# Performance work log

Hardware: AMD Instinct MI355X
Metric: run time of the kernel (lower is better)

## Reference

```python
import jax, jax.numpy as jnp
import numpy as np

HIDDEN = 1024
HEADS = 16
HEAD_DIM = HIDDEN // HEADS


def setup_inputs() -> dict:
    key = jax.random.key(0)
    ks = jax.random.split(key, 4)
    B, S, H = 2, 2048, HIDDEN
    scale = 1.0 / np.sqrt(H)
    return {
        "inputs": jax.random.normal(ks[0], (B, S, H), dtype=jnp.float32),
        "mask": jnp.ones((B, S), dtype=jnp.int32),
        "Wq": jax.random.normal(ks[1], (H, H), dtype=jnp.float32) * scale,
        "bq": jnp.zeros((H,), dtype=jnp.float32),
        "Wk": jax.random.normal(ks[2], (H, H), dtype=jnp.float32) * scale,
        "bk": jnp.zeros((H,), dtype=jnp.float32),
        "Wv": jax.random.normal(ks[3], (H, H), dtype=jnp.float32) * scale,
        "bv": jnp.zeros((H,), dtype=jnp.float32),
    }


def _split_heads(x, B, S):
    # [B,S,H] -> [B,heads,S,head_dim]
    return x.reshape(B, S, HEADS, HEAD_DIM).transpose(0, 2, 1, 3)


def reference(inputs, mask, Wq, bq, Wk, bk, Wv, bv):
    B, S, H = inputs.shape
    q = _split_heads(inputs @ Wq.T + bq, B, S)
    k = _split_heads(inputs @ Wk.T + bk, B, S)
    v = _split_heads(inputs @ Wv.T + bv, B, S)
    scores = jnp.einsum("bhqd,bhkd->bhqk", q, k) / jnp.sqrt(
        jnp.asarray(HEAD_DIM, dtype=inputs.dtype))
    # mask broadcast [B,1,1,S]; zeros -> -inf
    scores = jnp.where(mask[:, None, None, :] == 0, -jnp.inf, scores)
    attn = jax.nn.softmax(scores, axis=-1)
    context = jnp.einsum("bhqk,bhkd->bhqd", attn, v)
    return context.transpose(0, 2, 1, 3).reshape(B, S, H)
```

## Files before the change

### kernel.cpp

```cpp
#include <hip/hip_runtime.h>
#include <hip/hip_fp16.h>

constexpr int S_LEN  = 2048;
constexpr int HID    = 1024;
constexpr int HEADS  = 16;
constexpr int HDIM   = 64;
constexpr int BATCH  = 2;
constexpr int BH     = BATCH * HEADS;
constexpr int M_ROWS = BATCH * S_LEN;

typedef _Float16 half8  __attribute__((ext_vector_type(8)));
typedef _Float16 half4v __attribute__((ext_vector_type(4)));
typedef _Float16 half2v __attribute__((ext_vector_type(2)));
typedef float    f32x4  __attribute__((ext_vector_type(4)));
typedef float    f32x16 __attribute__((ext_vector_type(16)));
typedef unsigned uint4v __attribute__((ext_vector_type(4)));

constexpr float EXP2_OFF = -11.541560327111707f;
constexpr float Q_SCALE  = 0.18033688011112042f;

__global__ __launch_bounds__(256) void cvt_kernel(
    const float* __restrict__ X,  const float* __restrict__ Wq,
    const float* __restrict__ Wk, const float* __restrict__ Wv,
    const int* __restrict__ mask,
    _Float16* __restrict__ Xh,  _Float16* __restrict__ Wqh,
    _Float16* __restrict__ Wkh, _Float16* __restrict__ Wvh,
    float* __restrict__ maskF)
{
    const int blk = blockIdx.x;
    if (blk >= 3584) {
        const int loc = blk - 3584;
        const size_t e = ((size_t)loc * 256 + threadIdx.x) * 8;
        #pragma unroll
        for (int i = 0; i < 8; ++i)
            maskF[e + i] = mask[e + i] ? EXP2_OFF : -1.0e30f;
        return;
    }
    const float* src; _Float16* dst; int loc;
    if (blk < 2048)      { src = X;  dst = Xh;  loc = blk; }
    else if (blk < 2560) { src = Wq; dst = Wqh; loc = blk - 2048; }
    else if (blk < 3072) { src = Wk; dst = Wkh; loc = blk - 2560; }
    else                 { src = Wv; dst = Wvh; loc = blk - 3072; }
    const size_t e = ((size_t)loc * 256 + threadIdx.x) * 8;
    float4 a = *reinterpret_cast<const float4*>(&src[e]);
    float4 b = *reinterpret_cast<const float4*>(&src[e + 4]);
    half8 h = { (_Float16)a.x, (_Float16)a.y, (_Float16)a.z, (_Float16)a.w,
                (_Float16)b.x, (_Float16)b.y, (_Float16)b.z, (_Float16)b.w };
    *reinterpret_cast<half8*>(&dst[e]) = h;
}

__device__ __forceinline__ void async_cp16(_Float16* lds, const _Float16* g) {
    __builtin_amdgcn_global_load_lds(
        (const __attribute__((address_space(1))) void*)g,
        (__attribute__((address_space(3))) void*)lds, 16, 0, 0);
}
__device__ __forceinline__ void async_cp4(float* lds, const float* g) {
    __builtin_amdgcn_global_load_lds(
        (const __attribute__((address_space(1))) void*)g,
        (__attribute__((address_space(3))) void*)lds, 4, 0, 0);
}

__device__ __forceinline__ void permlane32_swap(unsigned &x, unsigned &y) {
    asm("v_permlane32_swap_b32 %0, %1" : "+v"(x), "+v"(y));
}

__global__ __launch_bounds__(256) void qkv_proj_kernel(
    const _Float16* __restrict__ Xh,
    const _Float16* __restrict__ Wqh, const _Float16* __restrict__ Wkh,
    const _Float16* __restrict__ Wvh,
    const float* __restrict__ bq, const float* __restrict__ bk,
    const float* __restrict__ bv,
    _Float16* __restrict__ Qo, _Float16* __restrict__ Ko,
    _Float16* __restrict__ Vt)
{
    const int mode = blockIdx.z;
    const _Float16* W    = (mode == 0) ? Wqh : (mode == 1) ? Wkh : Wvh;
    const float*    bias = (mode == 0) ? bq  : (mode == 1) ? bk  : bv;

    const int m0 = blockIdx.x * 128, n0 = blockIdx.y * 128;
    const int tid = threadIdx.x, wave = tid >> 6, lane = tid & 63;
    const int l31 = lane & 31, kg = lane >> 5;

    __shared__ _Float16 SMEM[18432];

    f32x16 acc[2][2];
    #pragma unroll
    for (int mt = 0; mt < 2; ++mt)
        #pragma unroll
        for (int nt = 0; nt < 2; ++nt)
            #pragma unroll
            for (int i = 0; i < 16; ++i) acc[mt][nt][i] = 0.f;

    const int wm = (wave & 1) * 64, wn = (wave >> 1) * 64;

    const int srow = tid >> 2, spos = tid & 3;
    auto stage = [&](int k0, int b) {
        _Float16* Asb = SMEM + b * 8192;
        _Float16* Bsb = Asb + 4096;
        #pragma unroll
        for (int j = 0; j < 2; ++j) {
            const int row = srow + j * 64;
            const int sch = spos ^ (row & 3);
            async_cp16(&Asb[j * 2048 + tid * 8],
                       &Xh[(size_t)(m0 + row) * HID + k0 + sch * 8]);
            async_cp16(&Bsb[j * 2048 + tid * 8],
                       &W [(size_t)(n0 + row) * HID + k0 + sch * 8]);
        }
    };

    stage(0, 0);
    int buf = 0;

    for (int k0 = 0; k0 < HID; k0 += 32) {
        __syncthreads();
        if (k0 + 32 < HID) stage(k0 + 32, buf ^ 1);
        _Float16* Asb = SMEM + buf * 8192;
        _Float16* Bsb = Asb + 4096;

        #pragma unroll
        for (int c = 0; c < 2; ++c) {
            const int k8 = c * 2 + kg;
            half8 af[2], bf[2];
            #pragma unroll
            for (int mt = 0; mt < 2; ++mt) {
                const int row = wm + mt * 32 + l31;
                af[mt] = *reinterpret_cast<const half8*>(
                    &Asb[row * 32 + ((k8 ^ (row & 3)) * 8)]);
            }
            #pragma unroll
            for (int nt = 0; nt < 2; ++nt) {
                const int row = wn + nt * 32 + l31;
                bf[nt] = *reinterpret_cast<const half8*>(
                    &Bsb[row * 32 + ((k8 ^ (row & 3)) * 8)]);
            }
            #pragma unroll
            for (int mt = 0; mt < 2; ++mt)
                #pragma unroll
                for (int nt = 0; nt < 2; ++nt)
                    acc[mt][nt] = __builtin_amdgcn_mfma_f32_32x32x16_f16(
                        af[mt], bf[nt], acc[mt][nt], 0, 0, 0);
        }
        buf ^= 1;
    }
    __syncthreads();

    _Float16* T = SMEM + wave * 4608;

    const int nn  = n0 + wn;
    const int hh  = nn >> 6;
    const int mm  = m0 + wm;
    const int bb  = mm >> 11;
    const int bhv = bb * HEADS + hh;
    const int s0  = mm & 2047;
    const int rowg = lane >> 3, chunk = lane & 7;

    if (mode < 2) {
        _Float16* Out = (mode == 0) ? Qo : Ko;
        #pragma unroll
        for (int nt = 0; nt < 2; ++nt) {
            const int col = nt * 32 + l31;
            float bias_n = bias[nn + col];
            #pragma unroll
            for (int mt = 0; mt < 2; ++mt)
                #pragma unroll
                for (int r = 0; r < 16; ++r) {
                    const int row_l = (r & 3) + 8 * (r >> 2) + 4 * kg;
                    float v = acc[mt][nt][r] + bias_n;
                    if (mode == 0) v *= Q_SCALE;
                    T[(mt * 32 + row_l) * 72 + col] = (_Float16)v;
                }
        }
        asm volatile("s_waitcnt lgkmcnt(0)" ::: "memory");
        #pragma unroll
        for (int j = 0; j < 8; ++j) {
            const int sr = j * 8 + rowg;
            half8 v = *reinterpret_cast<const half8*>(&T[sr * 72 + chunk * 8]);
            *reinterpret_cast<half8*>(
                &Out[((size_t)bhv * S_LEN + s0 + sr) * HDIM + chunk * 8]) = v;
        }
    } else {
        #pragma unroll
        for (int nt = 0; nt < 2; ++nt) {
            const int col = nt * 32 + l31;
            const float bias_n = bias[nn + col];
            #pragma unroll
            for (int mt = 0; mt < 2; ++mt)
                #pragma unroll
                for (int rg = 0; rg < 4; ++rg) {
                    half4v t = { (_Float16)(acc[mt][nt][rg * 4 + 0] + bias_n),
                                 (_Float16)(acc[mt][nt][rg * 4 + 1] + bias_n),
                                 (_Float16)(acc[mt][nt][rg * 4 + 2] + bias_n),
                                 (_Float16)(acc[mt][nt][rg * 4 + 3] + bias_n) };
                    const int s_off = mt * 32 + 8 * rg + 4 * kg;
                    *reinterpret_cast<half4v*>(&T[col * 72 + s_off]) = t;
                }
        }
        asm volatile("s_waitcnt lgkmcnt(0)" ::: "memory");
        #pragma unroll
        for (int j = 0; j < 8; ++j) {
            const int dr = j * 8 + rowg;
            half8 v = *reinterpret_cast<const half8*>(&T[dr * 72 + chunk * 8]);
            *reinterpret_cast<half8*>(
                &Vt[((size_t)bhv * HDIM + dr) * S_LEN + s0 + chunk * 8]) = v;
        }
    }
}

__global__ __launch_bounds__(512, 4) void attn_kernel(
    const _Float16* __restrict__ Q, const _Float16* __restrict__ K,
    const _Float16* __restrict__ Vt, const float* __restrict__ maskF,
    float* __restrict__ Out)
{
    const int id   = blockIdx.x;
    const int xcd  = id & 7;
    const int bh   = xcd * 4 + ((id >> 3) & 3);
    const int qt   = id >> 5;
    const int b = bh >> 4, h = bh & 15;
    const int tid = threadIdx.x, wave = tid >> 6, lane = tid & 63;
    const int l31 = lane & 31, kg = lane >> 5;
    const int wq = wave & 3, wk = wave >> 2;

    __shared__ _Float16 SMEM[3 * 8192];
    __shared__ float    Ms[3][8][64];

    const _Float16* Qb = Q  + (size_t)bh * S_LEN * HDIM;
    const _Float16* Kb = K  + (size_t)bh * S_LEN * HDIM;
    const _Float16* Vb = Vt + (size_t)bh * HDIM * S_LEN;
    const float*    mb = maskF + b * S_LEN;

    const int qrow = qt * 128 + wq * 32 + l31;

    half8 qf[4];
    #pragma unroll
    for (int kc = 0; kc < 4; ++kc)
        qf[kc] = *reinterpret_cast<const half8*>(
            &Qb[(size_t)qrow * HDIM + kc * 16 + kg * 8]);
    asm volatile("s_waitcnt vmcnt(0)" ::: "memory");

    f32x16 acc[2];
    #pragma unroll
    for (int dt = 0; dt < 2; ++dt)
        #pragma unroll
        for (int i = 0; i < 16; ++i) acc[dt][i] = 0.f;
    float den = 0.f;

    const int srow = tid >> 3;
    const int slot = tid & 7;
    auto stage = [&](int tile, int bufsel) {
        const int kb   = tile * 64;
        const int csrc = slot ^ (srow & 7);
        _Float16* Kd = SMEM + bufsel * 8192;
        _Float16* Vd = Kd + 4096;
        async_cp16(&Kd[tid * 8], &Kb[(size_t)(kb + srow) * HDIM + csrc * 8]);
        async_cp16(&Vd[tid * 8], &Vb[(size_t)srow * S_LEN + kb + csrc * 8]);
        async_cp4(&Ms[bufsel][wave][lane], &mb[kb + lane]);
    };

    constexpr int NT = S_LEN / 64;
    stage(0, 0);
    stage(1, 1);
    int buf = 0;
    const int rsw = l31 & 7;

    for (int t = 0; t < NT; ++t) {
        asm volatile("s_waitcnt vmcnt(3)" ::: "memory");
        __builtin_amdgcn_s_barrier();
        asm volatile("" ::: "memory");

        {
            int nt2 = t + 2; if (nt2 >= NT) nt2 -= NT;
            int nb  = buf + 2; if (nb >= 3) nb -= 3;
            stage(nt2, nb);
        }

        const _Float16* Kl = SMEM + buf * 8192;
        const _Float16* Vl = Kl + 4096;
        const float*    Mw = Ms[buf][wave];

        float4 mm0 = *reinterpret_cast<const float4*>(&Mw[wk * 32 + 0 + kg * 4]);
        float4 mm1 = *reinterpret_cast<const float4*>(&Mw[wk * 32 + 8 + kg * 4]);
        float4 mm2 = *reinterpret_cast<const float4*>(&Mw[wk * 32 + 16 + kg * 4]);
        float4 mm3 = *reinterpret_cast<const float4*>(&Mw[wk * 32 + 24 + kg * 4]);
        f32x16 sc = { mm0.x, mm0.y, mm0.z, mm0.w,
                      mm1.x, mm1.y, mm1.z, mm1.w,
                      mm2.x, mm2.y, mm2.z, mm2.w,
                      mm3.x, mm3.y, mm3.z, mm3.w };

        const _Float16* Krow = &Kl[(wk * 32 + l31) * 64];
        half8 kf[4];
        #pragma unroll
        for (int kc = 0; kc < 4; ++kc)
            kf[kc] = *reinterpret_cast<const half8*>(
                &Krow[((kc * 2 + kg) ^ rsw) * 8]);
        __builtin_amdgcn_s_setprio(1);
        #pragma unroll
        for (int kc = 0; kc < 4; ++kc)
            sc = __builtin_amdgcn_mfma_f32_32x32x16_f16(kf[kc], qf[kc], sc, 0, 0, 0);
        __builtin_amdgcn_s_setprio(0);

        half8 vf[2][2];
        #pragma unroll
        for (int dt = 0; dt < 2; ++dt) {
            const _Float16* Vrow = &Vl[(dt * 32 + l31) * 64];
            #pragma unroll
            for (int hh = 0; hh < 2; ++hh)
                vf[dt][hh] = *reinterpret_cast<const half8*>(
                    &Vrow[((wk * 4 + hh * 2 + kg) ^ rsw) * 8]);
        }

        float p[16];
        #pragma unroll
        for (int r = 0; r < 16; ++r)
            p[r] = __builtin_amdgcn_exp2f(sc[r]);
        den += (((p[0] + p[1]) + (p[2] + p[3])) +
                ((p[4] + p[5]) + (p[6] + p[7]))) +
               (((p[8] + p[9]) + (p[10] + p[11])) +
                ((p[12] + p[13]) + (p[14] + p[15])));

        #pragma unroll
        for (int hh = 0; hh < 2; ++hh) {
            unsigned a0 = __builtin_bit_cast(unsigned,
                __builtin_amdgcn_cvt_pkrtz(p[hh * 8 + 0], p[hh * 8 + 1]));
            unsigned a1 = __builtin_bit_cast(unsigned,
                __builtin_amdgcn_cvt_pkrtz(p[hh * 8 + 2], p[hh * 8 + 3]));
            unsigned b0 = __builtin_bit_cast(unsigned,
                __builtin_amdgcn_cvt_pkrtz(p[hh * 8 + 4], p[hh * 8 + 5]));
            unsigned b1 = __builtin_bit_cast(unsigned,
                __builtin_amdgcn_cvt_pkrtz(p[hh * 8 + 6], p[hh * 8 + 7]));
            permlane32_swap(a0, b0);
            permlane32_swap(a1, b1);
            uint4v pd = { a0, a1, b0, b1 };
            half8 pf = __builtin_bit_cast(half8, pd);
            __builtin_amdgcn_s_setprio(1);
            acc[0] = __builtin_amdgcn_mfma_f32_32x32x16_f16(
                vf[0][hh], pf, acc[0], 0, 0, 0);
            acc[1] = __builtin_amdgcn_mfma_f32_32x32x16_f16(
                vf[1][hh], pf, acc[1], 0, 0, 0);
            __builtin_amdgcn_s_setprio(0);
        }
        if (++buf == 3) buf = 0;
    }

    asm volatile("s_waitcnt vmcnt(0)" ::: "memory");
    __syncthreads();

    den += __shfl_xor(den, 32, 64);

    float* LF = reinterpret_cast<float*>(SMEM);
    float* DF = reinterpret_cast<float*>(Ms);
    if (wk == 1) {
        float* wbase = LF + (wq * 64 + lane) * 36;
        #pragma unroll
        for (int dt = 0; dt < 2; ++dt)
            #pragma unroll
            for (int g = 0; g < 4; ++g) {
                float4 o = { acc[dt][g * 4 + 0], acc[dt][g * 4 + 1],
                             acc[dt][g * 4 + 2], acc[dt][g * 4 + 3] };
                *reinterpret_cast<float4*>(&wbase[dt * 16 + g * 4]) = o;
            }
        if (kg == 0) DF[wq * 32 + l31] = den;
    }
    __syncthreads();
    if (wk == 0) {
        const float* rbase = LF + (wq * 64 + lane) * 36;
        const float inv = 1.0f / (den + DF[wq * 32 + l31]);
        float* orow = Out + ((size_t)(b * S_LEN + qrow)) * HID + h * HDIM;
        #pragma unroll
        for (int dt = 0; dt < 2; ++dt)
            #pragma unroll
            for (int g = 0; g < 4; ++g) {
                float4 pv = *reinterpret_cast<const float4*>(
                    &rbase[dt * 16 + g * 4]);
                float4 o = { (acc[dt][g * 4 + 0] + pv.x) * inv,
                             (acc[dt][g * 4 + 1] + pv.y) * inv,
                             (acc[dt][g * 4 + 2] + pv.z) * inv,
                             (acc[dt][g * 4 + 3] + pv.w) * inv };
                *reinterpret_cast<float4*>(&orow[dt * 32 + g * 8 + kg * 4]) = o;
            }
    }
}

extern "C" void kernel_launch(void* const* d_in, const int* in_sizes, int n_in,
                              void* d_out, int out_size, void* d_ws, size_t ws_size,
                              hipStream_t stream) {
    const float* X  = (const float*)d_in[0];
    const int*   mk = (const int*)  d_in[1];
    const float* Wq = (const float*)d_in[2];
    const float* bq = (const float*)d_in[3];
    const float* Wk = (const float*)d_in[4];
    const float* bk = (const float*)d_in[5];
    const float* Wv = (const float*)d_in[6];
    const float* bv = (const float*)d_in[7];
    float* out = (float*)d_out;

    _Float16* Xh  = (_Float16*)d_ws;
    _Float16* Wqh = Xh  + (size_t)M_ROWS * HID;
    _Float16* Wkh = Wqh + (size_t)HID * HID;
    _Float16* Wvh = Wkh + (size_t)HID * HID;
    _Float16* Q   = Wvh + (size_t)HID * HID;
    _Float16* K   = Q   + (size_t)BH * S_LEN * HDIM;
    _Float16* Vt  = K   + (size_t)BH * S_LEN * HDIM;
    float*    maskF = (float*)(Vt + (size_t)BH * S_LEN * HDIM);

    cvt_kernel<<<3586, 256, 0, stream>>>(X, Wq, Wk, Wv, mk, Xh, Wqh, Wkh, Wvh, maskF);

    dim3 gp(M_ROWS / 128, HID / 128, 3);
    qkv_proj_kernel<<<gp, 256, 0, stream>>>(Xh, Wqh, Wkh, Wvh, bq, bk, bv, Q, K, Vt);

    attn_kernel<<<512, 512, 0, stream>>>(Q, K, Vt, maskF, out);
}
```

Baseline: 169.0 us.

## Triple-buffer QKV GEMM staging and load mask bias into registers directly

The projection GEMM moves from a double-buffered loop with __syncthreads to a three-stage LDS ring with vmcnt-based waits and raised MFMA priority, so global loads run further ahead of compute. The attention kernel no longer stages the mask through LDS via 4-byte async copies. Each thread instead prefetches its mask-bias float4s for the next tile into registers, one iteration ahead, and the vmcnt thresholds are adjusted to match. This cuts LDS traffic and small async copies but adds register pressure and more LDS use in the GEMM, which may reduce occupancy.

```diff
diff --git a/kernel.cpp b/kernel.cpp
--- a/kernel.cpp
+++ b/kernel.cpp
@@ -54,11 +54,6 @@
         (const __attribute__((address_space(1))) void*)g,
         (__attribute__((address_space(3))) void*)lds, 16, 0, 0);
 }
-__device__ __forceinline__ void async_cp4(float* lds, const float* g) {
-    __builtin_amdgcn_global_load_lds(
-        (const __attribute__((address_space(1))) void*)g,
-        (__attribute__((address_space(3))) void*)lds, 4, 0, 0);
-}
 
 __device__ __forceinline__ void permlane32_swap(unsigned &x, unsigned &y) {
     asm("v_permlane32_swap_b32 %0, %1" : "+v"(x), "+v"(y));
@@ -81,7 +76,7 @@
     const int tid = threadIdx.x, wave = tid >> 6, lane = tid & 63;
     const int l31 = lane & 31, kg = lane >> 5;
 
-    __shared__ _Float16 SMEM[18432];
+    __shared__ _Float16 SMEM[24576];
 
     f32x16 acc[2][2];
     #pragma unroll
@@ -108,12 +103,22 @@
         }
     };
 
+    constexpr int NIT = HID / 32;
     stage(0, 0);
+    stage(32, 1);
     int buf = 0;
 
-    for (int k0 = 0; k0 < HID; k0 += 32) {
-        __syncthreads();
-        if (k0 + 32 < HID) stage(k0 + 32, buf ^ 1);
+    for (int it = 0; it < NIT; ++it) {
+        asm volatile("s_waitcnt vmcnt(4)" ::: "memory");
+        __builtin_amdgcn_s_barrier();
+        asm volatile("" ::: "memory");
+
+        {
+            int it2 = it + 2; if (it2 >= NIT) it2 -= NIT;
+            int nb  = buf + 2; if (nb >= 3) nb -= 3;
+            stage(it2 * 32, nb);
+        }
+
         _Float16* Asb = SMEM + buf * 8192;
         _Float16* Bsb = Asb + 4096;
 
@@ -133,15 +138,18 @@
                 bf[nt] = *reinterpret_cast<const half8*>(
                     &Bsb[row * 32 + ((k8 ^ (row & 3)) * 8)]);
             }
+            __builtin_amdgcn_s_setprio(1);
             #pragma unroll
             for (int mt = 0; mt < 2; ++mt)
                 #pragma unroll
                 for (int nt = 0; nt < 2; ++nt)
                     acc[mt][nt] = __builtin_amdgcn_mfma_f32_32x32x16_f16(
                         af[mt], bf[nt], acc[mt][nt], 0, 0, 0);
-        }
-        buf ^= 1;
-    }
+            __builtin_amdgcn_s_setprio(0);
+        }
+        if (++buf == 3) buf = 0;
+    }
+    asm volatile("s_waitcnt vmcnt(0)" ::: "memory");
     __syncthreads();
 
     _Float16* T = SMEM + wave * 4608;
@@ -221,12 +229,12 @@
     const int wq = wave & 3, wk = wave >> 2;
 
     __shared__ _Float16 SMEM[3 * 8192];
-    __shared__ float    Ms[3][8][64];
 
     const _Float16* Qb = Q  + (size_t)bh * S_LEN * HDIM;
     const _Float16* Kb = K  + (size_t)bh * S_LEN * HDIM;
     const _Float16* Vb = Vt + (size_t)bh * HDIM * S_LEN;
     const float*    mb = maskF + b * S_LEN;
+    const float*    mwk = mb + wk * 32 + kg * 4;
 
     const int qrow = qt * 128 + wq * 32 + l31;
 
@@ -250,23 +258,38 @@
         const int kb   = tile * 64;
         const int csrc = slot ^ (srow & 7);
         _Float16* Kd = SMEM + bufsel * 8192;
-        _Float16* Vd = Kd + 4096;
         async_cp16(&Kd[tid * 8], &Kb[(size_t)(kb + srow) * HDIM + csrc * 8]);
-        async_cp16(&Vd[tid * 8], &Vb[(size_t)srow * S_LEN + kb + csrc * 8]);
-        async_cp4(&Ms[bufsel][wave][lane], &mb[kb + lane]);
+        async_cp16(&Kd[4096 + tid * 8],
+                   &Vb[(size_t)srow * S_LEN + kb + csrc * 8]);
     };
 
     constexpr int NT = S_LEN / 64;
+    float4 cmC[4], cmN[4];
+
     stage(0, 0);
+    asm volatile("" ::: "memory");
+    #pragma unroll
+    for (int g = 0; g < 4; ++g)
+        cmC[g] = *reinterpret_cast<const float4*>(&mwk[g * 8]);
+    asm volatile("" ::: "memory");
     stage(1, 1);
+
     int buf = 0;
     const int rsw = l31 & 7;
 
     for (int t = 0; t < NT; ++t) {
-        asm volatile("s_waitcnt vmcnt(3)" ::: "memory");
+        asm volatile("s_waitcnt vmcnt(2)" ::: "memory");
         __builtin_amdgcn_s_barrier();
         asm volatile("" ::: "memory");
 
+        {
+            const int tn = (t + 1) & (NT - 1);
+            const float* mp = mwk + tn * 64;
+            #pragma unroll
+            for (int g = 0; g < 4; ++g)
+                cmN[g] = *reinterpret_cast<const float4*>(&mp[g * 8]);
+        }
+        asm volatile("" ::: "memory");
         {
             int nt2 = t + 2; if (nt2 >= NT) nt2 -= NT;
             int nb  = buf + 2; if (nb >= 3) nb -= 3;
@@ -275,16 +298,11 @@
 
         const _Float16* Kl = SMEM + buf * 8192;
         const _Float16* Vl = Kl + 4096;
-        const float*    Mw = Ms[buf][wave];
-
-        float4 mm0 = *reinterpret_cast<const float4*>(&Mw[wk * 32 + 0 + kg * 4]);
-        float4 mm1 = *reinterpret_cast<const float4*>(&Mw[wk * 32 + 8 + kg * 4]);
-        float4 mm2 = *reinterpret_cast<const float4*>(&Mw[wk * 32 + 16 + kg * 4]);
-        float4 mm3 = *reinterpret_cast<const float4*>(&Mw[wk * 32 + 24 + kg * 4]);
-        f32x16 sc = { mm0.x, mm0.y, mm0.z, mm0.w,
-                      mm1.x, mm1.y, mm1.z, mm1.w,
-                      mm2.x, mm2.y, mm2.z, mm2.w,
-                      mm3.x, mm3.y, mm3.z, mm3.w };
+
+        f32x16 sc = { cmC[0].x, cmC[0].y, cmC[0].z, cmC[0].w,
+                      cmC[1].x, cmC[1].y, cmC[1].z, cmC[1].w,
+                      cmC[2].x, cmC[2].y, cmC[2].z, cmC[2].w,
+                      cmC[3].x, cmC[3].y, cmC[3].z, cmC[3].w };
 
         const _Float16* Krow = &Kl[(wk * 32 + l31) * 64];
         half8 kf[4];
@@ -338,6 +356,9 @@
                 vf[1][hh], pf, acc[1], 0, 0, 0);
             __builtin_amdgcn_s_setprio(0);
         }
+
+        #pragma unroll
+        for (int g = 0; g < 4; ++g) cmC[g] = cmN[g];
         if (++buf == 3) buf = 0;
     }
 
@@ -347,7 +368,7 @@
     den += __shfl_xor(den, 32, 64);
 
     float* LF = reinterpret_cast<float*>(SMEM);
-    float* DF = reinterpret_cast<float*>(Ms);
+    float* DF = LF + 9216;
     if (wk == 1) {
         float* wbase = LF + (wq * 64 + lane) * 36;
         #pragma unroll
```

Result: slower. 173.7 us (+2.8%).

## Triple-buffer QKV projection loads and change attention LDS swizzle

Applied to the files above, without the earlier changes.

The QKV projection GEMM moves from double-buffered staging with a full __syncthreads per k-step to a three-stage ring. It prefetches two tiles ahead, waits with a partial vmcnt before a raw barrier, and raises wave priority around the MFMA block, so global loads overlap compute better. Shared memory grows to hold the third buffer. The attention kernel's K/V LDS swizzle key changes from row&7 to a row+row/8 based XOR, with per-wave and per-dt offsets, to reduce bank conflicts on the fragment reads.

```diff
diff --git a/kernel.cpp b/kernel.cpp
--- a/kernel.cpp
+++ b/kernel.cpp
@@ -81,7 +81,7 @@
     const int tid = threadIdx.x, wave = tid >> 6, lane = tid & 63;
     const int l31 = lane & 31, kg = lane >> 5;
 
-    __shared__ _Float16 SMEM[18432];
+    __shared__ _Float16 SMEM[24576];
 
     f32x16 acc[2][2];
     #pragma unroll
@@ -108,12 +108,22 @@
         }
     };
 
+    constexpr int NIT = HID / 32;
     stage(0, 0);
+    stage(32, 1);
     int buf = 0;
 
-    for (int k0 = 0; k0 < HID; k0 += 32) {
-        __syncthreads();
-        if (k0 + 32 < HID) stage(k0 + 32, buf ^ 1);
+    for (int it = 0; it < NIT; ++it) {
+        asm volatile("s_waitcnt vmcnt(4)" ::: "memory");
+        __builtin_amdgcn_s_barrier();
+        asm volatile("" ::: "memory");
+
+        {
+            int it2 = it + 2; if (it2 >= NIT) it2 -= NIT;
+            int nb  = buf + 2; if (nb >= 3) nb -= 3;
+            stage(it2 * 32, nb);
+        }
+
         _Float16* Asb = SMEM + buf * 8192;
         _Float16* Bsb = Asb + 4096;
 
@@ -133,15 +143,18 @@
                 bf[nt] = *reinterpret_cast<const half8*>(
                     &Bsb[row * 32 + ((k8 ^ (row & 3)) * 8)]);
             }
+            __builtin_amdgcn_s_setprio(1);
             #pragma unroll
             for (int mt = 0; mt < 2; ++mt)
                 #pragma unroll
                 for (int nt = 0; nt < 2; ++nt)
                     acc[mt][nt] = __builtin_amdgcn_mfma_f32_32x32x16_f16(
                         af[mt], bf[nt], acc[mt][nt], 0, 0, 0);
-        }
-        buf ^= 1;
-    }
+            __builtin_amdgcn_s_setprio(0);
+        }
+        if (++buf == 3) buf = 0;
+    }
+    asm volatile("s_waitcnt vmcnt(0)" ::: "memory");
     __syncthreads();
 
     _Float16* T = SMEM + wave * 4608;
@@ -246,13 +259,14 @@
 
     const int srow = tid >> 3;
     const int slot = tid & 7;
+    const int gs   = (srow + (srow >> 3)) & 7;
     auto stage = [&](int tile, int bufsel) {
         const int kb   = tile * 64;
-        const int csrc = slot ^ (srow & 7);
+        const int csrc = slot ^ gs;
         _Float16* Kd = SMEM + bufsel * 8192;
-        _Float16* Vd = Kd + 4096;
         async_cp16(&Kd[tid * 8], &Kb[(size_t)(kb + srow) * HDIM + csrc * 8]);
-        async_cp16(&Vd[tid * 8], &Vb[(size_t)srow * S_LEN + kb + csrc * 8]);
+        async_cp16(&Kd[4096 + tid * 8],
+                   &Vb[(size_t)srow * S_LEN + kb + csrc * 8]);
         async_cp4(&Ms[bufsel][wave][lane], &mb[kb + lane]);
     };
 
@@ -260,7 +274,9 @@
     stage(0, 0);
     stage(1, 1);
     int buf = 0;
-    const int rsw = l31 & 7;
+    const int gkey = (l31 + (l31 >> 3) + 4 * wk) & 7;
+    const int gv0  = (l31 + (l31 >> 3)) & 7;
+    const int gv1  = (gv0 + 4) & 7;
 
     for (int t = 0; t < NT; ++t) {
         asm volatile("s_waitcnt vmcnt(3)" ::: "memory");
@@ -291,7 +307,7 @@
         #pragma unroll
         for (int kc = 0; kc < 4; ++kc)
             kf[kc] = *reinterpret_cast<const half8*>(
-                &Krow[((kc * 2 + kg) ^ rsw) * 8]);
+                &Krow[((kc * 2 + kg) ^ gkey) * 8]);
         __builtin_amdgcn_s_setprio(1);
         #pragma unroll
         for (int kc = 0; kc < 4; ++kc)
@@ -302,10 +318,11 @@
         #pragma unroll
         for (int dt = 0; dt < 2; ++dt) {
             const _Float16* Vrow = &Vl[(dt * 32 + l31) * 64];
+            const int gv = dt ? gv1 : gv0;
             #pragma unroll
             for (int hh = 0; hh < 2; ++hh)
                 vf[dt][hh] = *reinterpret_cast<const half8*>(
-                    &Vrow[((wk * 4 + hh * 2 + kg) ^ rsw) * 8]);
+                    &Vrow[((wk * 4 + hh * 2 + kg) ^ gv) * 8]);
         }
 
         float p[16];
```

After: 171.3 us. Within noise of the previous version (+1.4%).
